# Performance work log

Measured on AMD Instinct MI355X. Metric: run time of the kernel, lower is better.

## Reference

```python
import jax, jax.numpy as jnp
import numpy as np

EPS = 1e-5  # torch.nn.LayerNorm default

def _layer_norm(h):
    # elementwise_affine=False LayerNorm over last dim
    mu = jnp.mean(h, axis=-1, keepdims=True)
    var = jnp.mean(jnp.square(h - mu), axis=-1, keepdims=True)
    return (h - mu) * jax.lax.rsqrt(var + EPS)

def setup_inputs() -> dict:
    key = jax.random.key(0)
    ks = jax.random.split(key, 5)
    N, D = 2048, 1024
    x = jax.random.normal(ks[0], (N, D), dtype=jnp.float32)
    scale = 0.02
    w_q = jax.random.normal(ks[1], (D, D), dtype=jnp.float32) * scale
    w_k = jax.random.normal(ks[2], (D, D), dtype=jnp.float32) * scale
    w_v = jax.random.normal(ks[3], (D, D), dtype=jnp.float32) * scale
    w_o = jax.random.normal(ks[4], (D, D), dtype=jnp.float32) * scale
    return {"x": x, "w_q": w_q, "w_k": w_k, "w_v": w_v, "w_o": w_o}

def reference(x, w_q, w_k, w_v, w_o):
    N, D = x.shape
    H = 16
    dh = D // H
    xn = _layer_norm(x)
    # per-head projections -> [H, N, dh]
    q = _layer_norm((xn @ w_q).reshape(N, H, dh)).astype(jnp.float16).transpose(1, 0, 2)
    k = _layer_norm((xn @ w_k).reshape(N, H, dh)).astype(jnp.float16).transpose(1, 0, 2)
    v = (xn @ w_v).reshape(N, H, dh).transpose(1, 0, 2)
    sm_scale = 1.0 / jnp.sqrt(jnp.float32(dh))  # flex_attention default scale
    scores = jnp.einsum('hqd,hkd->hqk', q, k, preferred_element_type=jnp.float32) * sm_scale
    # block-sparse pattern: q_idx // 16 == kv_idx % 16 (empty rows for q_idx >= 256)
    idx = jnp.arange(N)
    mask = (idx[:, None] // 16) == (idx[None, :] % 16)  # [N, N]
    neg = jnp.float32(-1e30)
    smax = jnp.max(jnp.where(mask, scores, neg), axis=-1, keepdims=True)
    p = jnp.where(mask, jnp.exp(scores - smax), 0.0)  # [H, N, N]
    denom = jnp.sum(p, axis=-1, keepdims=True)
    # flash-style semantics: fully masked rows output 0
    attn = jnp.einsum('hqk,hkd->hqd', p, v) / jnp.maximum(denom, 1e-30)
    outs = attn.transpose(1, 0, 2).reshape(N, D).astype(jnp.float32)
    return x + outs @ w_o
```

## Files before the change

### kernel.cpp

```cpp
#include <hip/hip_runtime.h>
#include <hip/hip_bf16.h>

typedef unsigned short u16;
typedef __attribute__((ext_vector_type(8))) __bf16 bf16x8;
typedef __attribute__((ext_vector_type(4))) float f32x4;
typedef __attribute__((ext_vector_type(4))) unsigned short u16x4;
typedef __attribute__((ext_vector_type(4))) unsigned int u32x4;

#define DEV static __device__ __forceinline__

static constexpr int N = 2048, D = 1024;
static constexpr float EPS = 1e-5f;

DEV u16 f2b(float f) {
  union { float f; unsigned u; } x; x.f = f;
  unsigned r = x.u + 0x7FFFu + ((x.u >> 16) & 1u);
  return (u16)(r >> 16);
}
DEV float b2f(u16 h) {
  union { unsigned u; float f; } x; x.u = ((unsigned)h) << 16;
  return x.f;
}

DEV void async16(const void* g, void* l) {
  __builtin_amdgcn_global_load_lds(
      (const __attribute__((address_space(1))) unsigned int*)g,
      (__attribute__((address_space(3))) unsigned int*)l, 16, 0, 0);
}

__global__ __launch_bounds__(256) void k_pre(const float* __restrict__ x,
                                             const float* __restrict__ wq, const float* __restrict__ wk,
                                             const float* __restrict__ wv, const float* __restrict__ wo,
                                             u16* __restrict__ xn, u16* __restrict__ wt,
                                             float* __restrict__ out) {
  const int t = threadIdx.x;
  if (blockIdx.x < 2048) {
    const int row = blockIdx.x;
    const float4 v = ((const float4*)(x + (size_t)row * D))[t];
    ((float4*)(out + (size_t)row * D))[t] = v;
    float s  = v.x + v.y + v.z + v.w;
    float ss = v.x * v.x + v.y * v.y + v.z * v.z + v.w * v.w;
    __shared__ float red0[4], red1[4];
    for (int off = 32; off; off >>= 1) { s += __shfl_xor(s, off, 64); ss += __shfl_xor(ss, off, 64); }
    const int w = t >> 6, l = t & 63;
    if (l == 0) { red0[w] = s; red1[w] = ss; }
    __syncthreads();
    s  = red0[0] + red0[1] + red0[2] + red0[3];
    ss = red1[0] + red1[1] + red1[2] + red1[3];
    const float mu = s * (1.0f / D);
    const float var = ss * (1.0f / D) - mu * mu;
    const float rs = rsqrtf(var + EPS);
    u16x4 o;
    o.x = f2b((v.x - mu) * rs); o.y = f2b((v.y - mu) * rs);
    o.z = f2b((v.z - mu) * rs); o.w = f2b((v.w - mu) * rs);
    ((u16x4*)(xn + (size_t)row * D))[t] = o;
  } else {
    const int bid = blockIdx.x - 2048;
    const int z = bid >> 10, rem = bid & 1023;
    const float* src = z == 0 ? wq : z == 1 ? wk : z == 2 ? wv : wo;
    u16* dst = wt + (size_t)z * D * D;
    __shared__ float tile[32][33];
    const int k0 = (rem >> 5) * 32, n0 = (rem & 31) * 32;
    const int c = t & 31, r4 = t >> 5;
#pragma unroll
    for (int p = 0; p < 4; ++p) { int r = r4 + p * 8; tile[r][c] = src[(size_t)(k0 + r) * D + n0 + c]; }
    __syncthreads();
#pragma unroll
    for (int p = 0; p < 4; ++p) { int r = r4 + p * 8; dst[(size_t)(n0 + r) * D + k0 + c] = f2b(tile[c][r]); }
  }
}

struct GS { u16 As[64 * 64]; u16 Bs[64 * 64]; };

template<int EPI>
DEV void gemm64(GS& sh, const u16* __restrict__ A, const u16* __restrict__ BT,
                void* __restrict__ dst, int row0, int col0, int dcol0, int ldc,
                int kbeg, int kend) {
  constexpr int K = 1024, BK = 64;
  const int t = threadIdx.x;
  const int w = t >> 6, l = t & 63;
  const int wm = w << 4;
  const int fr = l & 15, kg = l >> 4;
  const int rq = kg << 2;

  f32x4 acc[4];
#pragma unroll
  for (int j = 0; j < 4; ++j) acc[j] = (f32x4){0.f, 0.f, 0.f, 0.f};

  const int r0s = t >> 3,          cs0 = (t & 7) ^ (r0s & 7);
  const int r1s = (t + 256) >> 3,  cs1 = (t & 7) ^ (r1s & 7);
  const u16* gA0 = A  + (size_t)(row0 + r0s) * K + cs0 * 8;
  const u16* gA1 = A  + (size_t)(row0 + r1s) * K + cs1 * 8;
  const u16* gB0 = BT + (size_t)(col0 + r0s) * K + cs0 * 8;
  const u16* gB1 = BT + (size_t)(col0 + r1s) * K + cs1 * 8;
  u16* lA0 = &sh.As[t * 8];
  u16* lA1 = &sh.As[(t + 256) * 8];
  u16* lB0 = &sh.Bs[t * 8];
  u16* lB1 = &sh.Bs[(t + 256) * 8];

  for (int k0 = kbeg; k0 < kend; k0 += BK) {
    async16(gA0 + k0, lA0);
    async16(gA1 + k0, lA1);
    async16(gB0 + k0, lB0);
    async16(gB1 + k0, lB1);
    __syncthreads();
    bf16x8 af[2], bf[4][2];
#pragma unroll
    for (int kk = 0; kk < 2; ++kk)
      af[kk] = *(const bf16x8*)&sh.As[(wm + fr) * BK + ((kk * 4 + kg) ^ (fr & 7)) * 8];
#pragma unroll
    for (int j = 0; j < 4; ++j)
#pragma unroll
      for (int kk = 0; kk < 2; ++kk)
        bf[j][kk] = *(const bf16x8*)&sh.Bs[(j * 16 + fr) * BK + ((kk * 4 + kg) ^ (fr & 7)) * 8];
#pragma unroll
    for (int kk = 0; kk < 2; ++kk)
#pragma unroll
      for (int j = 0; j < 4; ++j)
        acc[j] = __builtin_amdgcn_mfma_f32_16x16x32_bf16(af[kk], bf[j][kk], acc[j], 0, 0, 0);
    __syncthreads();
  }

  if constexpr (EPI == 1) {
    float ps[4], pss[4];
#pragma unroll
    for (int r = 0; r < 4; ++r) {
      float s = 0.f, ss = 0.f;
#pragma unroll
      for (int j = 0; j < 4; ++j) { const float v = acc[j][r]; s += v; ss += v * v; }
      ps[r] = s; pss[r] = ss;
    }
    for (int off = 1; off < 16; off <<= 1)
#pragma unroll
      for (int r = 0; r < 4; ++r) {
        ps[r]  += __shfl_xor(ps[r],  off, 16);
        pss[r] += __shfl_xor(pss[r], off, 16);
      }
    u16* o = (u16*)dst;
#pragma unroll
    for (int r = 0; r < 4; ++r) {
      const float mu = ps[r] * (1.0f / 64);
      const float rs = rsqrtf(pss[r] * (1.0f / 64) - mu * mu + EPS);
      const int row = row0 + wm + rq + r;
#pragma unroll
      for (int j = 0; j < 4; ++j)
        o[(size_t)row * ldc + dcol0 + j * 16 + fr] = f2b((acc[j][r] - mu) * rs);
    }
  } else if constexpr (EPI == 2) {
    u16* o = (u16*)dst;
#pragma unroll
    for (int r = 0; r < 4; ++r) {
      const int row = row0 + wm + rq + r;
#pragma unroll
      for (int j = 0; j < 4; ++j)
        o[(size_t)row * ldc + dcol0 + j * 16 + fr] = f2b(acc[j][r]);
    }
  } else {
    float* o = (float*)dst;
#pragma unroll
    for (int r = 0; r < 4; ++r) {
      const int row = row0 + wm + rq + r;
#pragma unroll
      for (int j = 0; j < 4; ++j)
        atomicAdd(&o[(size_t)row * ldc + dcol0 + j * 16 + fr], acc[j][r]);
    }
  }
}

__global__ __launch_bounds__(256) void k_gemm_qkv(const u16* __restrict__ xn, const u16* __restrict__ wt,
                                                  u16* __restrict__ qh, u16* __restrict__ kh,
                                                  u16* __restrict__ vh) {
  __shared__ GS sh;
  const int bid = blockIdx.x;
  if (bid < 1024) {
    const int r0 = (bid >> 5) * 64, c0 = (bid & 31) * 64;
    const u16* BT = wt + (size_t)D * D;
    if (c0 < 1024) gemm64<1>(sh, xn, BT, kh, r0, c0, c0, D, 0, 1024);
    else           gemm64<2>(sh, xn, BT, vh, r0, c0, c0 - 1024, D, 0, 1024);
  } else {
    const int q = bid - 1024;
    gemm64<1>(sh, xn, wt, qh, (q >> 4) * 64, (q & 15) * 64, (q & 15) * 64, D, 0, 1024);
  }
}

__global__ __launch_bounds__(256) void k_gemm_o(const u16* __restrict__ attnb, const u16* __restrict__ wt,
                                                float* __restrict__ out) {
  __shared__ GS sh;
  const int s = blockIdx.x & 1, tile = blockIdx.x >> 1;
  gemm64<3>(sh, attnb, wt + (size_t)3 * D * D, out,
            (tile >> 4) * 64, (tile & 15) * 64, (tile & 15) * 64, D, s * 512, s * 512 + 512);
}

__global__ __launch_bounds__(256) void k_attn(const u16* __restrict__ qh, const u16* __restrict__ kh,
                                              const u16* __restrict__ vh, u16* __restrict__ attnb) {
  const int h = blockIdx.x >> 4, b = blockIdx.x & 15;
  __shared__ float q_s[16][68];
  __shared__ u16  k_u[128][72];
  __shared__ u16  v_u[128][64];
  __shared__ float s_s[16][132];
  __shared__ float inv_den[16];
  const int t = threadIdx.x;

  {
    const int i = t >> 4, sub = t & 15;
    const u16x4 qq = *(const u16x4*)&qh[(size_t)(b * 16 + i) * D + h * 64 + sub * 4];
    q_s[i][sub * 4 + 0] = b2f(qq.x); q_s[i][sub * 4 + 1] = b2f(qq.y);
    q_s[i][sub * 4 + 2] = b2f(qq.z); q_s[i][sub * 4 + 3] = b2f(qq.w);
  }
#pragma unroll
  for (int it = 0; it < 4; ++it) {
    const int idx = t + it * 256;
    const int j = idx >> 3, c = (idx & 7) * 8;
    const int kr = b + 16 * j;
    *(u32x4*)&k_u[j][c] = *(const u32x4*)&kh[(size_t)kr * D + h * 64 + c];
    *(u32x4*)&v_u[j][c] = *(const u32x4*)&vh[(size_t)kr * D + h * 64 + c];
  }
  __syncthreads();

  const int i = t >> 4;
  const int sub = t & 15;
#pragma unroll
  for (int jj = 0; jj < 8; ++jj) {
    const int j = sub + 16 * jj;
    float acc = 0.f;
#pragma unroll
    for (int d4 = 0; d4 < 16; ++d4) {
      const u16x4 kk = *(const u16x4*)&k_u[j][d4 * 4];
      acc += q_s[i][d4 * 4 + 0] * b2f(kk.x) + q_s[i][d4 * 4 + 1] * b2f(kk.y)
           + q_s[i][d4 * 4 + 2] * b2f(kk.z) + q_s[i][d4 * 4 + 3] * b2f(kk.w);
    }
    s_s[i][j] = acc * 0.125f;
  }
  __syncthreads();
  float m = -1e30f;
#pragma unroll
  for (int jj = 0; jj < 8; ++jj) m = fmaxf(m, s_s[i][sub + 16 * jj]);
  for (int off = 1; off < 16; off <<= 1) m = fmaxf(m, __shfl_xor(m, off, 64));
  float sum = 0.f;
#pragma unroll
  for (int jj = 0; jj < 8; ++jj) {
    const int j = sub + 16 * jj;
    const float p = __expf(s_s[i][j] - m);
    s_s[i][j] = p;
    sum += p;
  }
  for (int off = 1; off < 16; off <<= 1) sum += __shfl_xor(sum, off, 64);
  if (sub == 0) inv_den[i] = 1.0f / sum;
  __syncthreads();

  const int db = sub << 2;
  float a0 = 0, a1 = 0, a2 = 0, a3 = 0;
  for (int j = 0; j < 128; ++j) {
    const float p = s_s[i][j];
    const u16x4 vv = *(const u16x4*)&v_u[j][db];
    a0 += p * b2f(vv.x); a1 += p * b2f(vv.y); a2 += p * b2f(vv.z); a3 += p * b2f(vv.w);
  }
  const float inv = inv_den[i];
  u16x4 o;
  o.x = f2b(a0 * inv); o.y = f2b(a1 * inv); o.z = f2b(a2 * inv); o.w = f2b(a3 * inv);
  *(u16x4*)&attnb[(size_t)(b * 16 + i) * D + h * 64 + db] = o;
}

extern "C" void kernel_launch(void* const* d_in, const int* in_sizes, int n_in,
                              void* d_out, int out_size, void* d_ws, size_t ws_size,
                              hipStream_t stream) {
  const float* x  = (const float*)d_in[0];
  const float* wq = (const float*)d_in[1];
  const float* wk = (const float*)d_in[2];
  const float* wv = (const float*)d_in[3];
  const float* wo = (const float*)d_in[4];
  float* out = (float*)d_out;
  char* ws = (char*)d_ws;

  u16* xn    = (u16*)(ws + 0);
  u16* wt    = (u16*)(ws + 4194304);
  u16* qh    = (u16*)(ws + 12582912);
  u16* kh    = (u16*)(ws + 13107200);
  u16* vh    = (u16*)(ws + 17301504);
  u16* attnb = (u16*)(ws + 21495808);

  k_pre<<<dim3(6144), dim3(256), 0, stream>>>(x, wq, wk, wv, wo, xn, wt, out);
  k_gemm_qkv<<<dim3(1088), dim3(256), 0, stream>>>(xn, wt, qh, kh, vh);
  k_attn<<<dim3(256), dim3(256), 0, stream>>>(qh, kh, vh, attnb);
  k_gemm_o<<<dim3(128), dim3(256), 0, stream>>>(attnb, wt, out);
}
```

Baseline: 53.89 us.

## Double-buffer GEMM shared tiles and remap QKV block order across XCDs

Splits the GEMM LDS staging into two buffers so the async global-to-LDS copy of the next K tile is issued before computing on the current one, aiming to overlap memory latency with MFMA work. It also permutes block indices in the QKV GEMM (stride 136 over groups of 8) so neighbouring tiles land on the same XCD for better L2 reuse. Doubling LDS per block can lower occupancy. The loop relies on the end-of-iteration barrier to make the prefetched tile visible, which only holds if async16 completes before that barrier.

Measured after the change: 56.87 us. 1.06x slower.

```diff
diff --git a/kernel.cpp b/kernel.cpp
--- a/kernel.cpp
+++ b/kernel.cpp
@@ -70,7 +70,7 @@
   }
 }
 
-struct GS { u16 As[64 * 64]; u16 Bs[64 * 64]; };
+struct GS { u16 As[2][64 * 64]; u16 Bs[2][64 * 64]; };
 
 template<int EPI>
 DEV void gemm64(GS& sh, const u16* __restrict__ A, const u16* __restrict__ BT,
@@ -93,32 +93,40 @@
   const u16* gA1 = A  + (size_t)(row0 + r1s) * K + cs1 * 8;
   const u16* gB0 = BT + (size_t)(col0 + r0s) * K + cs0 * 8;
   const u16* gB1 = BT + (size_t)(col0 + r1s) * K + cs1 * 8;
-  u16* lA0 = &sh.As[t * 8];
-  u16* lA1 = &sh.As[(t + 256) * 8];
-  u16* lB0 = &sh.Bs[t * 8];
-  u16* lB1 = &sh.Bs[(t + 256) * 8];
-
+  const int ld0 = t * 8, ld1 = (t + 256) * 8;
+
+  async16(gA0 + kbeg, &sh.As[0][ld0]);
+  async16(gA1 + kbeg, &sh.As[0][ld1]);
+  async16(gB0 + kbeg, &sh.Bs[0][ld0]);
+  async16(gB1 + kbeg, &sh.Bs[0][ld1]);
+  __syncthreads();
+
+  int cur = 0;
   for (int k0 = kbeg; k0 < kend; k0 += BK) {
-    async16(gA0 + k0, lA0);
-    async16(gA1 + k0, lA1);
-    async16(gB0 + k0, lB0);
-    async16(gB1 + k0, lB1);
-    __syncthreads();
+    const int nxt = k0 + BK;
+    if (nxt < kend) {
+      const int o = cur ^ 1;
+      async16(gA0 + nxt, &sh.As[o][ld0]);
+      async16(gA1 + nxt, &sh.As[o][ld1]);
+      async16(gB0 + nxt, &sh.Bs[o][ld0]);
+      async16(gB1 + nxt, &sh.Bs[o][ld1]);
+    }
     bf16x8 af[2], bf[4][2];
 #pragma unroll
     for (int kk = 0; kk < 2; ++kk)
-      af[kk] = *(const bf16x8*)&sh.As[(wm + fr) * BK + ((kk * 4 + kg) ^ (fr & 7)) * 8];
+      af[kk] = *(const bf16x8*)&sh.As[cur][(wm + fr) * BK + (((kk << 2) + kg) ^ (fr & 7)) * 8];
 #pragma unroll
     for (int j = 0; j < 4; ++j)
 #pragma unroll
       for (int kk = 0; kk < 2; ++kk)
-        bf[j][kk] = *(const bf16x8*)&sh.Bs[(j * 16 + fr) * BK + ((kk * 4 + kg) ^ (fr & 7)) * 8];
+        bf[j][kk] = *(const bf16x8*)&sh.Bs[cur][(j * 16 + fr) * BK + (((kk << 2) + kg) ^ (fr & 7)) * 8];
 #pragma unroll
     for (int kk = 0; kk < 2; ++kk)
 #pragma unroll
       for (int j = 0; j < 4; ++j)
         acc[j] = __builtin_amdgcn_mfma_f32_16x16x32_bf16(af[kk], bf[j][kk], acc[j], 0, 0, 0);
     __syncthreads();
+    cur ^= 1;
   }
 
   if constexpr (EPI == 1) {
@@ -171,7 +179,7 @@
                                                   u16* __restrict__ qh, u16* __restrict__ kh,
                                                   u16* __restrict__ vh) {
   __shared__ GS sh;
-  const int bid = blockIdx.x;
+  const int bid = (blockIdx.x & 7) * 136 + (blockIdx.x >> 3);
   if (bid < 1024) {
     const int r0 = (bid >> 5) * 64, c0 = (bid & 31) * 64;
     const u16* BT = wt + (size_t)D * D;
```

## Use double-buffered 128x128 tiles for the K/V projection GEMM

Applied to the files above, without the earlier changes.

Adds a 128x128-tile GEMM path in which each wave computes a 64x64 sub-tile. It uses two LDS buffers with async prefetch two k-steps ahead and waits on vmcnt instead of a full sync. K and V projections now run as 256 large tiles in place of 1024 small ones, which raises data reuse per loaded tile and overlaps loads with MFMA work. Q keeps the 64x64 path, and the grid shrinks from 1088 to 320 blocks. The costs are more LDS and registers per block and fewer blocks than CUs, which may hurt occupancy.

Result: slower. 64.05 us (+18.9%).

```diff
diff --git a/kernel.cpp b/kernel.cpp
--- a/kernel.cpp
+++ b/kernel.cpp
@@ -70,7 +70,8 @@
   }
 }
 
-struct GS { u16 As[64 * 64]; u16 Bs[64 * 64]; };
+struct GS  { u16 As[64 * 64];  u16 Bs[64 * 64]; };
+struct GS2 { u16 As[2][128 * 64]; u16 Bs[2][128 * 64]; };
 
 template<int EPI>
 DEV void gemm64(GS& sh, const u16* __restrict__ A, const u16* __restrict__ BT,
@@ -93,26 +94,22 @@
   const u16* gA1 = A  + (size_t)(row0 + r1s) * K + cs1 * 8;
   const u16* gB0 = BT + (size_t)(col0 + r0s) * K + cs0 * 8;
   const u16* gB1 = BT + (size_t)(col0 + r1s) * K + cs1 * 8;
-  u16* lA0 = &sh.As[t * 8];
-  u16* lA1 = &sh.As[(t + 256) * 8];
-  u16* lB0 = &sh.Bs[t * 8];
-  u16* lB1 = &sh.Bs[(t + 256) * 8];
 
   for (int k0 = kbeg; k0 < kend; k0 += BK) {
-    async16(gA0 + k0, lA0);
-    async16(gA1 + k0, lA1);
-    async16(gB0 + k0, lB0);
-    async16(gB1 + k0, lB1);
+    async16(gA0 + k0, &sh.As[t * 8]);
+    async16(gA1 + k0, &sh.As[(t + 256) * 8]);
+    async16(gB0 + k0, &sh.Bs[t * 8]);
+    async16(gB1 + k0, &sh.Bs[(t + 256) * 8]);
     __syncthreads();
     bf16x8 af[2], bf[4][2];
 #pragma unroll
     for (int kk = 0; kk < 2; ++kk)
-      af[kk] = *(const bf16x8*)&sh.As[(wm + fr) * BK + ((kk * 4 + kg) ^ (fr & 7)) * 8];
+      af[kk] = *(const bf16x8*)&sh.As[(wm + fr) * BK + (((kk << 2) + kg) ^ (fr & 7)) * 8];
 #pragma unroll
     for (int j = 0; j < 4; ++j)
 #pragma unroll
       for (int kk = 0; kk < 2; ++kk)
-        bf[j][kk] = *(const bf16x8*)&sh.Bs[(j * 16 + fr) * BK + ((kk * 4 + kg) ^ (fr & 7)) * 8];
+        bf[j][kk] = *(const bf16x8*)&sh.Bs[(j * 16 + fr) * BK + (((kk << 2) + kg) ^ (fr & 7)) * 8];
 #pragma unroll
     for (int kk = 0; kk < 2; ++kk)
 #pragma unroll
@@ -167,19 +164,121 @@
   }
 }
 
+template<bool LN>
+DEV void gemm128(GS2& sh, const u16* __restrict__ A, const u16* __restrict__ BT,
+                 u16* __restrict__ dst, int row0, int col0, int dcol0, int ldc) {
+  constexpr int K = 1024, BK = 64, NT = 16;
+  const int t = threadIdx.x;
+  const int w = t >> 6, l = t & 63;
+  const int wr = (w >> 1) << 6, wc = (w & 1) << 6;
+  const int fr = l & 15, kg = l >> 4;
+
+  f32x4 acc[4][4];
+#pragma unroll
+  for (int i = 0; i < 4; ++i)
+#pragma unroll
+    for (int j = 0; j < 4; ++j) acc[i][j] = (f32x4){0.f, 0.f, 0.f, 0.f};
+
+  const u16* gA[4]; const u16* gB[4];
+#pragma unroll
+  for (int p = 0; p < 4; ++p) {
+    const int c = t + p * 256, row = c >> 3, sc = (c & 7) ^ (row & 7);
+    gA[p] = A  + (size_t)(row0 + row) * K + sc * 8;
+    gB[p] = BT + (size_t)(col0 + row) * K + sc * 8;
+  }
+  const int ldsOff = t * 8;
+
+#define STAGE128(buf, kt) do {                                        \
+    const int _k0 = (kt) * BK;                                        \
+    _Pragma("unroll")                                                 \
+    for (int p = 0; p < 4; ++p) async16(gA[p] + _k0, &sh.As[buf][ldsOff + p * 2048]); \
+    _Pragma("unroll")                                                 \
+    for (int p = 0; p < 4; ++p) async16(gB[p] + _k0, &sh.Bs[buf][ldsOff + p * 2048]); \
+  } while (0)
+
+  STAGE128(0, 0);
+  STAGE128(1, 1);
+
+  for (int it = 0; it < NT; ++it) {
+    if (it == NT - 1) asm volatile("s_waitcnt vmcnt(0)" ::: "memory");
+    else              asm volatile("s_waitcnt vmcnt(8)" ::: "memory");
+    __builtin_amdgcn_s_barrier();
+    const u16* As = sh.As[it & 1];
+    const u16* Bs = sh.Bs[it & 1];
+    bf16x8 af[4][2], bf[4][2];
+#pragma unroll
+    for (int i = 0; i < 4; ++i)
+#pragma unroll
+      for (int kk = 0; kk < 2; ++kk)
+        af[i][kk] = *(const bf16x8*)&As[(wr + i * 16 + fr) * BK + (((kk << 2) + kg) ^ (fr & 7)) * 8];
+#pragma unroll
+    for (int j = 0; j < 4; ++j)
+#pragma unroll
+      for (int kk = 0; kk < 2; ++kk)
+        bf[j][kk] = *(const bf16x8*)&Bs[(wc + j * 16 + fr) * BK + (((kk << 2) + kg) ^ (fr & 7)) * 8];
+#pragma unroll
+    for (int kk = 0; kk < 2; ++kk)
+#pragma unroll
+      for (int i = 0; i < 4; ++i)
+#pragma unroll
+        for (int j = 0; j < 4; ++j)
+          acc[i][j] = __builtin_amdgcn_mfma_f32_16x16x32_bf16(af[i][kk], bf[j][kk], acc[i][j], 0, 0, 0);
+    __builtin_amdgcn_s_barrier();
+    if (it + 2 < NT) STAGE128(it & 1, it + 2);
+  }
+#undef STAGE128
+
+#pragma unroll
+  for (int i = 0; i < 4; ++i) {
+    if constexpr (LN) {
+      float ps[4], pss[4];
+#pragma unroll
+      for (int r = 0; r < 4; ++r) {
+        float s = 0.f, ss = 0.f;
+#pragma unroll
+        for (int j = 0; j < 4; ++j) { const float v = acc[i][j][r]; s += v; ss += v * v; }
+        ps[r] = s; pss[r] = ss;
+      }
+      for (int off = 1; off < 16; off <<= 1)
+#pragma unroll
+        for (int r = 0; r < 4; ++r) {
+          ps[r]  += __shfl_xor(ps[r],  off, 16);
+          pss[r] += __shfl_xor(pss[r], off, 16);
+        }
+#pragma unroll
+      for (int r = 0; r < 4; ++r) {
+        const float mu = ps[r] * (1.0f / 64);
+        const float rs = rsqrtf(pss[r] * (1.0f / 64) - mu * mu + EPS);
+        const int row = row0 + wr + i * 16 + (kg << 2) + r;
+#pragma unroll
+        for (int j = 0; j < 4; ++j)
+          dst[(size_t)row * ldc + dcol0 + wc + j * 16 + fr] = f2b((acc[i][j][r] - mu) * rs);
+      }
+    } else {
+#pragma unroll
+      for (int r = 0; r < 4; ++r) {
+        const int row = row0 + wr + i * 16 + (kg << 2) + r;
+#pragma unroll
+        for (int j = 0; j < 4; ++j)
+          dst[(size_t)row * ldc + dcol0 + wc + j * 16 + fr] = f2b(acc[i][j][r]);
+      }
+    }
+  }
+}
+
 __global__ __launch_bounds__(256) void k_gemm_qkv(const u16* __restrict__ xn, const u16* __restrict__ wt,
                                                   u16* __restrict__ qh, u16* __restrict__ kh,
                                                   u16* __restrict__ vh) {
-  __shared__ GS sh;
+  __shared__ GS2 sh;
   const int bid = blockIdx.x;
-  if (bid < 1024) {
-    const int r0 = (bid >> 5) * 64, c0 = (bid & 31) * 64;
+  if (bid < 64) {
+    gemm64<1>(*(GS*)&sh, xn, wt, qh, (bid >> 4) * 64, (bid & 15) * 64, (bid & 15) * 64, D, 0, 1024);
+  } else {
+    const int tile = bid - 64;
+    const int r0 = (tile >> 4) * 128, c0 = (tile & 15) * 128;
     const u16* BT = wt + (size_t)D * D;
-    if (c0 < 1024) gemm64<1>(sh, xn, BT, kh, r0, c0, c0, D, 0, 1024);
-    else           gemm64<2>(sh, xn, BT, vh, r0, c0, c0 - 1024, D, 0, 1024);
-  } else {
-    const int q = bid - 1024;
-    gemm64<1>(sh, xn, wt, qh, (q >> 4) * 64, (q & 15) * 64, (q & 15) * 64, D, 0, 1024);
+    if (c0 < 1024) gemm128<true >(sh, xn, BT, kh, r0, c0, c0,        D);
+    else           gemm128<false>(sh, xn, BT, vh, r0, c0, c0 - 1024, D);
   }
 }
 
@@ -280,7 +379,7 @@
   u16* attnb = (u16*)(ws + 21495808);
 
   k_pre<<<dim3(6144), dim3(256), 0, stream>>>(x, wq, wk, wv, wo, xn, wt, out);
-  k_gemm_qkv<<<dim3(1088), dim3(256), 0, stream>>>(xn, wt, qh, kh, vh);
+  k_gemm_qkv<<<dim3(320), dim3(256), 0, stream>>>(xn, wt, qh, kh, vh);
   k_attn<<<dim3(256), dim3(256), 0, stream>>>(qh, kh, vh, attnb);
   k_gemm_o<<<dim3(128), dim3(256), 0, stream>>>(attnb, wt, out);
 }
```
